# Performance work log

Hardware: AMD Instinct MI355X
Metric: run time of the kernel (lower is better)

The kernel has to match this reference:

```python
import jax, jax.numpy as jnp
import numpy as np


def setup_inputs() -> dict:
    key = jax.random.key(0)
    ks = jax.random.split(key, 3)
    n = 4096
    return {
        "params_batch": jax.random.uniform(ks[0], (n, 15), dtype=jnp.float32),
        "W1": jax.random.normal(ks[1], (8, 32), dtype=jnp.float32) * 0.1,
        "b1": jnp.zeros((32,), dtype=jnp.float32),
        "ln_g": jnp.ones((32,), dtype=jnp.float32),
        "ln_b": jnp.zeros((32,), dtype=jnp.float32),
        "W2": jax.random.normal(ks[2], (32, 16), dtype=jnp.float32) * 0.1,
        "b2": jnp.zeros((16,), dtype=jnp.float32),
    }


def _pairwise_mean(p):
    # p: [n, 15]; returns [n, 8] mean of pairwise features over j != i
    n = p.shape[0]
    t, ra, dec, psi = p[:, 5], p[:, 3], p[:, 4], p[:, 7]
    dt = jnp.abs(t[:, None] - t[None, :])                      # [n, n]
    dra = jnp.abs(ra[:, None] - ra[None, :])
    ddec = jnp.abs(dec[:, None] - dec[None, :])
    sky_sep = jnp.sqrt(dra ** 2 + ddec ** 2)
    m1 = p[:, 0] * 95.0 + 5.0
    m2 = p[:, 1] * 95.0 + 5.0
    mc = (m1 * m2) ** 0.6 / (m1 + m2) ** 0.2                    # chirp mass [n]
    mass_sim = 1.0 / (1.0 + jnp.abs(mc[:, None] - mc[None, :]) / 30.0)
    f_isco = 220.0 / (m1 + m2)
    freq_ov = jnp.exp(-jnp.abs(f_isco[:, None] - f_isco[None, :]) / 100.0)
    dist = p[:, 2] * 2950.0 + 50.0
    dist_ratio = jnp.minimum(dist[:, None], dist[None, :]) / jnp.maximum(dist[:, None], dist[None, :])
    dpsi = jnp.abs(psi[:, None] - psi[None, :])
    feats = jnp.stack([dt, sky_sep, mass_sim, freq_ov, dist_ratio, dpsi, dra, ddec], axis=-1)  # [n, n, 8]
    # diagonal (j == i) contributions: zeros except mass_sim/freq_ov/dist_ratio == 1
    diag = jnp.array([0.0, 0.0, 1.0, 1.0, 1.0, 0.0, 0.0, 0.0], dtype=p.dtype)
    return (feats.sum(axis=1) - diag) / (n - 1)


def reference(params_batch, W1, b1, ln_g, ln_b, W2, b2):
    x = _pairwise_mean(params_batch)          # [n, 8]
    h = x @ W1 + b1                           # [n, 32]
    mu = h.mean(axis=-1, keepdims=True)
    var = h.var(axis=-1, keepdims=True)
    h = (h - mu) * jax.lax.rsqrt(var + 1e-5) * ln_g + ln_b
    h = jax.nn.gelu(h, approximate=False)     # torch GELU default (erf)
    return h @ W2 + b2                        # [n, 16]
```

## Files before the change

### kernel.cpp

```cpp
#include <hip/hip_runtime.h>
#include <math.h>

#define N       4096
#define NPARAM  15
#define NJ      32
#define IB      64
#define JPB     (N / NJ)
#define JPW     (JPB / 4)

typedef float f32x2 __attribute__((ext_vector_type(2)));

static __device__ __forceinline__ f32x2 abs2(f32x2 v) {
  return f32x2{fabsf(v.x), fabsf(v.y)};
}

__device__ __forceinline__ void derive_params(const float* __restrict__ r, float* o) {
  float m1 = fmaf(r[0], 95.0f, 5.0f);
  float m2 = fmaf(r[1], 95.0f, 5.0f);
  float msum = m1 + m2;
  float mc30 = __builtin_amdgcn_exp2f(
      0.6f * __builtin_amdgcn_logf(m1 * m2)
      - 0.2f * __builtin_amdgcn_logf(msum)
      - 4.906890595608519f);
  o[0] = r[5];
  o[1] = r[3];
  o[2] = r[4];
  o[3] = r[7];
  o[4] = mc30;
  o[5] = 3.1739290899556993f * __builtin_amdgcn_rcpf(msum);
  o[6] = __builtin_amdgcn_logf(fmaf(r[2], 2950.0f, 50.0f));
  o[7] = 0.0f;
}

template <bool PARTIAL>
__global__ __launch_bounds__(256, 8) void pairwise_kernel(
    const float* __restrict__ p, float* __restrict__ out) {
  __shared__ float4 sAB[JPB / 2];
  __shared__ float4 sCD[JPB / 2];
  __shared__ float4 sEF[JPB / 2];
  __shared__ float2 sG[JPB / 2];
  __shared__ float sacc[4 * IB * 8];
  int t    = threadIdx.x;
  int ib   = blockIdx.x;
  int jb   = blockIdx.y;
  int w    = t >> 6;
  int lane = t & 63;
  int i    = ib * IB + lane;

  if (t < JPB) {
    int j = jb * JPB + t;
    float o[8];
    derive_params(p + (size_t)j * NPARAM, o);
    int h = t >> 1, l = t & 1;
    ((float*)sAB)[h * 4 + l]     = o[0];
    ((float*)sAB)[h * 4 + 2 + l] = o[1];
    ((float*)sCD)[h * 4 + l]     = o[2];
    ((float*)sCD)[h * 4 + 2 + l] = o[3];
    ((float*)sEF)[h * 4 + l]     = o[4];
    ((float*)sEF)[h * 4 + 2 + l] = o[5];
    ((float*)sG)[h * 2 + l]      = o[6];
  }

  float pi[8];
  derive_params(p + (size_t)i * NPARAM, pi);
  float ti = pi[0], rai = pi[1], deci = pi[2], psii = pi[3];
  float mci = pi[4], fi = pi[5], di = pi[6];

  __syncthreads();

  f32x2 a_dt = {0.f, 0.f}, a_sky = {0.f, 0.f}, a_ms = {0.f, 0.f},
        a_fo = {0.f, 0.f}, a_dr = {0.f, 0.f}, a_ps = {0.f, 0.f},
        a_ra = {0.f, 0.f}, a_dc = {0.f, 0.f};

  int qbase = w * (JPW / 2);
#pragma unroll
  for (int q = 0; q < JPW / 2; q++) {
    float4 ab = sAB[qbase + q];
    float4 cd = sCD[qbase + q];
    float4 ef = sEF[qbase + q];
    float2 g  = sG[qbase + q];
    f32x2 tj  = {ab.x, ab.y}, raj = {ab.z, ab.w};
    f32x2 dcj = {cd.x, cd.y}, psj = {cd.z, cd.w};
    f32x2 mcj = {ef.x, ef.y}, fj  = {ef.z, ef.w};
    f32x2 dj  = {g.x, g.y};

    f32x2 dra  = rai - raj;
    f32x2 ddec = deci - dcj;
    a_dt += abs2(ti - tj);
    a_ps += abs2(psii - psj);
    a_ra += abs2(dra);
    a_dc += abs2(ddec);
    f32x2 ss = dra * dra + ddec * ddec;
    a_sky += f32x2{__builtin_amdgcn_sqrtf(ss.x), __builtin_amdgcn_sqrtf(ss.y)};
    f32x2 u = 1.0f + abs2(mci - mcj);
    a_ms += f32x2{__builtin_amdgcn_rcpf(u.x), __builtin_amdgcn_rcpf(u.y)};
    f32x2 e1 = abs2(fi - fj);
    a_fo += f32x2{__builtin_amdgcn_exp2f(-e1.x), __builtin_amdgcn_exp2f(-e1.y)};
    f32x2 e2 = abs2(di - dj);
    a_dr += f32x2{__builtin_amdgcn_exp2f(-e2.x), __builtin_amdgcn_exp2f(-e2.y)};
  }

  float s0 = a_dt.x + a_dt.y;
  float s1 = a_sky.x + a_sky.y;
  float s2 = a_ms.x + a_ms.y;
  float s3 = a_fo.x + a_fo.y;
  float s4 = a_dr.x + a_dr.y;
  float s5 = a_ps.x + a_ps.y;
  float s6 = a_ra.x + a_ra.y;
  float s7 = a_dc.x + a_dc.y;

  float4* d = (float4*)(sacc + ((size_t)w * IB + lane) * 8);
  d[0] = make_float4(s0, s1, s2, s3);
  d[1] = make_float4(s4, s5, s6, s7);
  __syncthreads();

#pragma unroll
  for (int k = 0; k < 2; k++) {
    int pidx = t + k * 256;
    float v = sacc[pidx] + sacc[512 + pidx] + sacc[1024 + pidx] + sacc[1536 + pidx];
    if (PARTIAL) {
      out[((size_t)jb * N + (size_t)ib * IB) * 8 + pidx] = v;
    } else {
      atomicAdd(&out[((size_t)ib * IB) * 8 + pidx], v);
    }
  }
}

template <int SLICES>
__global__ __launch_bounds__(256) void mlp_kernel(
    const float* __restrict__ X,
    const float* __restrict__ W1, const float* __restrict__ b1,
    const float* __restrict__ ln_g, const float* __restrict__ ln_b,
    const float* __restrict__ W2, const float* __restrict__ b2,
    float* __restrict__ out) {
  __shared__ float sW1[8 * 32], sW2[32 * 16];
  __shared__ float sb1[32], sg[32], sbb[32], sb2[16];
  __shared__ float sx[16 * 8];
  __shared__ float sh[16 * 32];
  __shared__ float stmp[256];
  int t = threadIdx.x;
  sW1[t] = W1[t];
  sW2[t] = W2[t];
  sW2[t + 256] = W2[t + 256];
  if (t < 32) { sb1[t] = b1[t]; sg[t] = ln_g[t]; sbb[t] = ln_b[t]; }
  if (t < 16) sb2[t] = b2[t];

  int i0 = blockIdx.x * 16;

  {
    int r = t >> 4;
    int q = (t >> 3) & 1;
    int f = t & 7;
    float s = 0.f;
    if (SLICES == 1) {
      if (q == 0) s = X[(size_t)(i0 + r) * 8 + f];
    } else {
      const float* src = X + ((size_t)(q * (SLICES / 2)) * N + (i0 + r)) * 8 + f;
#pragma unroll
      for (int k = 0; k < SLICES / 2; k++) s += src[(size_t)k * N * 8];
    }
    stmp[t] = s;
    __syncthreads();
    if (q == 0) sx[r * 8 + f] = stmp[t] + stmp[t + 8];
  }
  __syncthreads();

  {
    int r = t >> 4;
    int u = t & 15;
    const float diag[8] = {0.f, 0.f, 1.f, 1.f, 1.f, 0.f, 0.f, 0.f};
    const float inv_nm1 = 1.0f / (float)(N - 1);
    float x[8];
#pragma unroll
    for (int k = 0; k < 8; k++) x[k] = (sx[r * 8 + k] - diag[k]) * inv_nm1;

    int o0 = u * 2, o1 = o0 + 1;
    float h0 = sb1[o0], h1 = sb1[o1];
#pragma unroll
    for (int k = 0; k < 8; k++) {
      h0 += x[k] * sW1[k * 32 + o0];
      h1 += x[k] * sW1[k * 32 + o1];
    }

    float sum = h0 + h1;
#pragma unroll
    for (int m = 1; m < 16; m <<= 1) sum += __shfl_xor(sum, m);
    float mu = sum * (1.0f / 32.0f);
    float d0 = h0 - mu, d1 = h1 - mu;
    float vs = d0 * d0 + d1 * d1;
#pragma unroll
    for (int m = 1; m < 16; m <<= 1) vs += __shfl_xor(vs, m);
    float inv = rsqrtf(vs * (1.0f / 32.0f) + 1e-5f);

    float hn0 = d0 * inv * sg[o0] + sbb[o0];
    float hn1 = d1 * inv * sg[o1] + sbb[o1];
    float g0 = 0.5f * hn0 * (1.0f + erff(hn0 * 0.70710678118654752f));
    float g1 = 0.5f * hn1 * (1.0f + erff(hn1 * 0.70710678118654752f));
    sh[r * 32 + o0] = g0;
    sh[r * 32 + o1] = g1;
    __syncthreads();

    float a = sb2[u];
#pragma unroll
    for (int k = 0; k < 32; k++) a += sh[r * 32 + k] * sW2[k * 16 + u];
    out[(size_t)(i0 + r) * 16 + u] = a;
  }
}

extern "C" void kernel_launch(void* const* d_in, const int* in_sizes, int n_in,
                              void* d_out, int out_size, void* d_ws, size_t ws_size,
                              hipStream_t stream) {
  const float* p    = (const float*)d_in[0];
  const float* W1   = (const float*)d_in[1];
  const float* b1   = (const float*)d_in[2];
  const float* ln_g = (const float*)d_in[3];
  const float* ln_b = (const float*)d_in[4];
  const float* W2   = (const float*)d_in[5];
  const float* b2   = (const float*)d_in[6];
  float* out = (float*)d_out;
  float* ws  = (float*)d_ws;

  const size_t need_partial = (size_t)NJ * N * 8 * sizeof(float);
  dim3 grid(N / IB, NJ);
  if (ws_size >= need_partial) {
    pairwise_kernel<true><<<grid, 256, 0, stream>>>(p, ws);
    mlp_kernel<NJ><<<N / 16, 256, 0, stream>>>(ws, W1, b1, ln_g, ln_b, W2, b2, out);
  } else {
    hipMemsetAsync(ws, 0, (size_t)N * 8 * sizeof(float), stream);
    pairwise_kernel<false><<<grid, 256, 0, stream>>>(p, ws);
    mlp_kernel<1><<<N / 16, 256, 0, stream>>>(ws, W1, b1, ln_g, ln_b, W2, b2, out);
  }
}
```

Before: 82.02 us.

## Precompute derived params in separate kernel and stream j-data from global

Adds a derive kernel that computes per-point derived parameters once, into a paired layout for j and a per-i layout. The pairwise kernel then reads j data directly from global memory as vectors instead of staging it in shared memory. This removes the shared-memory fill, one barrier and the redundant per-block transcendental derivation. The cost is an extra kernel launch and global or cache loads inside the inner loop. A 16-slice fallback is also added for smaller workspaces.

```diff
diff --git a/kernel.cpp b/kernel.cpp
--- a/kernel.cpp
+++ b/kernel.cpp
@@ -3,16 +3,10 @@
 
 #define N       4096
 #define NPARAM  15
-#define NJ      32
 #define IB      64
-#define JPB     (N / NJ)
-#define JPW     (JPB / 4)
 
 typedef float f32x2 __attribute__((ext_vector_type(2)));
-
-static __device__ __forceinline__ f32x2 abs2(f32x2 v) {
-  return f32x2{fabsf(v.x), fabsf(v.y)};
-}
+typedef float f32x4 __attribute__((ext_vector_type(4)));
 
 __device__ __forceinline__ void derive_params(const float* __restrict__ r, float* o) {
   float m1 = fmaf(r[0], 95.0f, 5.0f);
@@ -32,72 +26,80 @@
   o[7] = 0.0f;
 }
 
-template <bool PARTIAL>
+__global__ __launch_bounds__(256) void derive_kernel(
+    const float* __restrict__ p, float* __restrict__ Dpair,
+    float* __restrict__ Di) {
+  int j = blockIdx.x * 256 + threadIdx.x;
+  float o[8];
+  derive_params(p + (size_t)j * NPARAM, o);
+  f32x4* di = (f32x4*)(Di + (size_t)j * 8);
+  di[0] = f32x4{o[0], o[1], o[2], o[3]};
+  di[1] = f32x4{o[4], o[5], o[6], 0.0f};
+  float* dq = Dpair + (size_t)(j >> 1) * 16;
+  int l = j & 1;
+#pragma unroll
+  for (int k = 0; k < 7; k++) dq[k * 2 + l] = o[k];
+  if (l) { dq[14] = 0.0f; dq[15] = 0.0f; }
+}
+
+template <int NJT, bool PARTIAL>
 __global__ __launch_bounds__(256, 8) void pairwise_kernel(
-    const float* __restrict__ p, float* __restrict__ out) {
-  __shared__ float4 sAB[JPB / 2];
-  __shared__ float4 sCD[JPB / 2];
-  __shared__ float4 sEF[JPB / 2];
-  __shared__ float2 sG[JPB / 2];
+    const float* __restrict__ Dpair, const float* __restrict__ Di,
+    float* __restrict__ out) {
+  constexpr int JPB = N / NJT;
+  constexpr int JPW = JPB / 4;
   __shared__ float sacc[4 * IB * 8];
   int t    = threadIdx.x;
   int ib   = blockIdx.x;
   int jb   = blockIdx.y;
-  int w    = t >> 6;
+  int w    = __builtin_amdgcn_readfirstlane(t >> 6);
   int lane = t & 63;
   int i    = ib * IB + lane;
 
-  if (t < JPB) {
-    int j = jb * JPB + t;
-    float o[8];
-    derive_params(p + (size_t)j * NPARAM, o);
-    int h = t >> 1, l = t & 1;
-    ((float*)sAB)[h * 4 + l]     = o[0];
-    ((float*)sAB)[h * 4 + 2 + l] = o[1];
-    ((float*)sCD)[h * 4 + l]     = o[2];
-    ((float*)sCD)[h * 4 + 2 + l] = o[3];
-    ((float*)sEF)[h * 4 + l]     = o[4];
-    ((float*)sEF)[h * 4 + 2 + l] = o[5];
-    ((float*)sG)[h * 2 + l]      = o[6];
-  }
-
-  float pi[8];
-  derive_params(p + (size_t)i * NPARAM, pi);
-  float ti = pi[0], rai = pi[1], deci = pi[2], psii = pi[3];
-  float mci = pi[4], fi = pi[5], di = pi[6];
-
-  __syncthreads();
+  const f32x4* di = (const f32x4*)(Di + (size_t)i * 8);
+  f32x4 piA = di[0];
+  f32x4 piB = di[1];
+  float ti = piA.x, rai = piA.y, deci = piA.z, psii = piA.w;
+  float mci = piB.x, fi = piB.y, dsi = piB.z;
+
+  const float* dp = Dpair + ((size_t)jb * (JPB / 2) + (size_t)w * (JPW / 2)) * 16;
 
   f32x2 a_dt = {0.f, 0.f}, a_sky = {0.f, 0.f}, a_ms = {0.f, 0.f},
         a_fo = {0.f, 0.f}, a_dr = {0.f, 0.f}, a_ps = {0.f, 0.f},
         a_ra = {0.f, 0.f}, a_dc = {0.f, 0.f};
 
-  int qbase = w * (JPW / 2);
 #pragma unroll
   for (int q = 0; q < JPW / 2; q++) {
-    float4 ab = sAB[qbase + q];
-    float4 cd = sCD[qbase + q];
-    float4 ef = sEF[qbase + q];
-    float2 g  = sG[qbase + q];
-    f32x2 tj  = {ab.x, ab.y}, raj = {ab.z, ab.w};
-    f32x2 dcj = {cd.x, cd.y}, psj = {cd.z, cd.w};
-    f32x2 mcj = {ef.x, ef.y}, fj  = {ef.z, ef.w};
-    f32x2 dj  = {g.x, g.y};
-
-    f32x2 dra  = rai - raj;
-    f32x2 ddec = deci - dcj;
-    a_dt += abs2(ti - tj);
-    a_ps += abs2(psii - psj);
-    a_ra += abs2(dra);
-    a_dc += abs2(ddec);
-    f32x2 ss = dra * dra + ddec * ddec;
-    a_sky += f32x2{__builtin_amdgcn_sqrtf(ss.x), __builtin_amdgcn_sqrtf(ss.y)};
-    f32x2 u = 1.0f + abs2(mci - mcj);
-    a_ms += f32x2{__builtin_amdgcn_rcpf(u.x), __builtin_amdgcn_rcpf(u.y)};
-    f32x2 e1 = abs2(fi - fj);
-    a_fo += f32x2{__builtin_amdgcn_exp2f(-e1.x), __builtin_amdgcn_exp2f(-e1.y)};
-    f32x2 e2 = abs2(di - dj);
-    a_dr += f32x2{__builtin_amdgcn_exp2f(-e2.x), __builtin_amdgcn_exp2f(-e2.y)};
+    const f32x4* c4 = (const f32x4*)(dp + (size_t)q * 16);
+    f32x4 v0 = c4[0];
+    f32x4 v1 = c4[1];
+    f32x4 v2 = c4[2];
+    f32x4 v3 = c4[3];
+
+    f32x2 dt  = {ti - v0.x,   ti - v0.y};
+    f32x2 dra = {rai - v0.z,  rai - v0.w};
+    f32x2 ddc = {deci - v1.x, deci - v1.y};
+    f32x2 dps = {psii - v1.z, psii - v1.w};
+    a_dt.x += fabsf(dt.x);   a_dt.y += fabsf(dt.y);
+    a_ps.x += fabsf(dps.x);  a_ps.y += fabsf(dps.y);
+    a_ra.x += fabsf(dra.x);  a_ra.y += fabsf(dra.y);
+    a_dc.x += fabsf(ddc.x);  a_dc.y += fabsf(ddc.y);
+
+    f32x2 ss = dra * dra + ddc * ddc;
+    a_sky.x += __builtin_amdgcn_sqrtf(ss.x);
+    a_sky.y += __builtin_amdgcn_sqrtf(ss.y);
+
+    f32x2 dm = {mci - v2.x, mci - v2.y};
+    a_ms.x += __builtin_amdgcn_rcpf(1.0f + fabsf(dm.x));
+    a_ms.y += __builtin_amdgcn_rcpf(1.0f + fabsf(dm.y));
+
+    f32x2 df = {fi - v2.z, fi - v2.w};
+    a_fo.x += __builtin_amdgcn_exp2f(-fabsf(df.x));
+    a_fo.y += __builtin_amdgcn_exp2f(-fabsf(df.y));
+
+    f32x2 dd = {dsi - v3.x, dsi - v3.y};
+    a_dr.x += __builtin_amdgcn_exp2f(-fabsf(dd.x));
+    a_dr.y += __builtin_amdgcn_exp2f(-fabsf(dd.y));
   }
 
   float s0 = a_dt.x + a_dt.y;
@@ -220,14 +222,28 @@
   float* out = (float*)d_out;
   float* ws  = (float*)d_ws;
 
-  const size_t need_partial = (size_t)NJ * N * 8 * sizeof(float);
-  dim3 grid(N / IB, NJ);
-  if (ws_size >= need_partial) {
-    pairwise_kernel<true><<<grid, 256, 0, stream>>>(p, ws);
-    mlp_kernel<NJ><<<N / 16, 256, 0, stream>>>(ws, W1, b1, ln_g, ln_b, W2, b2, out);
+  float* Dpair = ws;
+  float* Di    = ws + 32768;
+  float* part  = ws + 65536;
+
+  const size_t base    = 65536 * sizeof(float);
+  const size_t need32  = base + (size_t)32 * N * 8 * sizeof(float);
+  const size_t need16  = base + (size_t)16 * N * 8 * sizeof(float);
+
+  derive_kernel<<<N / 256, 256, 0, stream>>>(p, Dpair, Di);
+
+  if (ws_size >= need32) {
+    dim3 grid(N / IB, 32);
+    pairwise_kernel<32, true><<<grid, 256, 0, stream>>>(Dpair, Di, part);
+    mlp_kernel<32><<<N / 16, 256, 0, stream>>>(part, W1, b1, ln_g, ln_b, W2, b2, out);
+  } else if (ws_size >= need16) {
+    dim3 grid(N / IB, 16);
+    pairwise_kernel<16, true><<<grid, 256, 0, stream>>>(Dpair, Di, part);
+    mlp_kernel<16><<<N / 16, 256, 0, stream>>>(part, W1, b1, ln_g, ln_b, W2, b2, out);
   } else {
-    hipMemsetAsync(ws, 0, (size_t)N * 8 * sizeof(float), stream);
-    pairwise_kernel<false><<<grid, 256, 0, stream>>>(p, ws);
-    mlp_kernel<1><<<N / 16, 256, 0, stream>>>(ws, W1, b1, ln_g, ln_b, W2, b2, out);
-  }
-}
+    hipMemsetAsync(part, 0, (size_t)N * 8 * sizeof(float), stream);
+    dim3 grid(N / IB, 32);
+    pairwise_kernel<32, false><<<grid, 256, 0, stream>>>(Dpair, Di, part);
+    mlp_kernel<1><<<N / 16, 256, 0, stream>>>(part, W1, b1, ln_g, ln_b, W2, b2, out);
+  }
+}
```

Result: slower. 173.9 us (+112.0%).
